# Optimization experiments

Measured on AMD Instinct MI355X. Metric: run time of the kernel, lower is better.

The kernel has to match this reference:

```python
import jax, jax.numpy as jnp
import numpy as np

EPS = 1e-5
NEG_SLOPE = 0.2

def _bn(x, gamma, beta):
    # BatchNorm1d in training mode: stats over (batch, length) per channel. x: [B,C,N]
    m = jnp.mean(x, axis=(0, 2), keepdims=True)
    v = jnp.mean((x - m) ** 2, axis=(0, 2), keepdims=True)  # biased variance
    return (x - m) * jax.lax.rsqrt(v + EPS) * gamma[None, :, None] + beta[None, :, None]

def setup_inputs() -> dict:
    key = jax.random.key(0)
    ks = jax.random.split(key, 7)
    B, C, N, H = 32, 64, 2048, 128
    s = 1.0 / np.sqrt(C)
    return {
        "x": jax.random.normal(ks[0], (B, C, N), dtype=jnp.float32),
        "wq": jax.random.normal(ks[1], (C, C), dtype=jnp.float32) * s,
        "wk": jax.random.normal(ks[2], (C, C), dtype=jnp.float32) * s,
        "wv": jax.random.normal(ks[3], (C, C), dtype=jnp.float32) * s,
        "w_ff1": jax.random.normal(ks[4], (H, C), dtype=jnp.float32) * s,
        "w_ff2": jax.random.normal(ks[5], (C, H), dtype=jnp.float32) * (1.0 / np.sqrt(H)),
        "bn1_gamma": jnp.ones((C,), dtype=jnp.float32),
        "bn1_beta": jnp.zeros((C,), dtype=jnp.float32),
        "bn2_gamma": jnp.ones((C,), dtype=jnp.float32),
        "bn2_beta": jnp.zeros((C,), dtype=jnp.float32),
    }

def reference(x, wq, wk, wv, w_ff1, w_ff2, bn1_gamma, bn1_beta, bn2_gamma, bn2_beta):
    # x: [B, C, N]; 1x1 convs are per-point channel matmuls
    C = x.shape[1]
    q = jnp.einsum('oc,bcn->bno', wq, x)          # [B,N,C]
    k = jnp.einsum('oc,bcn->bon', wk, x)          # [B,C,N]
    v = jnp.einsum('oc,bcn->bno', wv, x)          # [B,N,C] (v^T)
    energy = jnp.einsum('bnc,bcm->bnm', q, k)     # [B,N,N]
    attention = jax.nn.softmax(energy / jnp.sqrt(jnp.float32(C)), axis=-1)
    x_r = jnp.einsum('bnm,bmc->bcn', attention, v)  # [B,C,N]
    h = _bn(x + x_r, bn1_gamma, bn1_beta)
    ff = jnp.einsum('hc,bcn->bhn', w_ff1, h)      # [B,H,N]
    ff = jnp.where(ff >= 0, ff, NEG_SLOPE * ff)   # LeakyReLU(0.2)
    ff = jnp.einsum('ch,bhn->bcn', w_ff2, ff)     # [B,C,N]
    return _bn(h + ff, bn2_gamma, bn2_beta)
```

## Files before the change

### kernel.cpp

```cpp
#include <hip/hip_runtime.h>

#define B_ 32
#define C_ 64
#define N_ 2048
#define H_ 128

typedef unsigned short u16;
typedef unsigned int u32;
typedef float f32x4 __attribute__((ext_vector_type(4)));
typedef float f32x16 __attribute__((ext_vector_type(16)));
typedef __bf16 bf16x8 __attribute__((ext_vector_type(8)));
typedef __bf16 bf16x4 __attribute__((ext_vector_type(4)));
typedef unsigned short u16x4 __attribute__((ext_vector_type(4)));
typedef unsigned int u32x4v __attribute__((ext_vector_type(4)));

#define MFMA(a, b, c) __builtin_amdgcn_mfma_f32_16x16x32_bf16(a, b, c, 0, 0, 0)
#define MFMA32(a, b, c) __builtin_amdgcn_mfma_f32_32x32x16_bf16(a, b, c, 0, 0, 0)
#define EXP2(x) __builtin_amdgcn_exp2f(x)
#define LOG2E 1.44269504088896f

__device__ __forceinline__ int swz(int row, int cb) { return row * 128 + (cb ^ ((row & 7) << 4)); }
__device__ __forceinline__ int swz256(int row, int cb) { return row * 256 + (cb ^ ((row & 7) << 4)); }

__device__ __forceinline__ float b2f(u16 v) {
    union { u32 u; float f; } x; x.u = ((u32)v) << 16; return x.f;
}

__device__ __forceinline__ u32 cvtpk(float lo, float hi) {
    u32 r;
    asm("v_cvt_pk_bf16_f32 %0, %1, %2" : "=v"(r) : "v"(lo), "v"(hi));
    return r;
}

__device__ __forceinline__ bf16x8 pfrag(float p0, float p1, float p2, float p3,
                                        float p4, float p5, float p6, float p7) {
    u32 x1 = cvtpk(p0, p1), x2 = cvtpk(p2, p3);
    u32 y1 = cvtpk(p4, p5), y2 = cvtpk(p6, p7);
    asm volatile("v_permlane32_swap_b32 %0, %1" : "+v"(x1), "+v"(y1));
    asm volatile("v_permlane32_swap_b32 %0, %1" : "+v"(x2), "+v"(y2));
    u32x4v d; d[0] = x1; d[1] = x2; d[2] = y1; d[3] = y2;
    return __builtin_bit_cast(bf16x8, d);
}

__device__ __forceinline__ bf16x8 cvt8(const float* p, float s) {
    f32x4 a = *(const f32x4*)p, b = *(const f32x4*)(p + 4);
    bf16x8 o;
    o[0] = (__bf16)(a[0] * s); o[1] = (__bf16)(a[1] * s);
    o[2] = (__bf16)(a[2] * s); o[3] = (__bf16)(a[3] * s);
    o[4] = (__bf16)(b[0] * s); o[5] = (__bf16)(b[1] * s);
    o[6] = (__bf16)(b[2] * s); o[7] = (__bf16)(b[3] * s);
    return o;
}

__global__ __launch_bounds__(256) void qkv_k(
    const float* __restrict__ x,
    const float* __restrict__ wq, const float* __restrict__ wk, const float* __restrict__ wv,
    const float* __restrict__ w1, const float* __restrict__ w2,
    u16* __restrict__ Qg, u16* __restrict__ Kg, u16* __restrict__ Vg,
    u16* __restrict__ w1b, u16* __restrict__ w2b)
{
    const int b = blockIdx.y, nt = blockIdx.x, t = threadIdx.x;
    const int lane = t & 63, wave = t >> 6, g = lane >> 4, r16 = lane & 15;
    __shared__ __align__(16) u16 xT[128 * 64];
    const int n0 = nt * 128;

    bf16x8 wqf[4][2], wkf[4][2], wvf[4][2];
#pragma unroll
    for (int jt = 0; jt < 4; ++jt)
#pragma unroll
        for (int kc = 0; kc < 2; ++kc) {
            const int ro = (r16 + 16 * jt) * 64 + 8 * g + 32 * kc;
            wqf[jt][kc] = cvt8(wq + ro, 0.125f * LOG2E);
            wkf[jt][kc] = cvt8(wk + ro, 1.0f);
            wvf[jt][kc] = cvt8(wv + ro, 1.0f);
        }

    {
        int c = t >> 5;
        const int nn = (t & 31) * 4;
#pragma unroll
        for (int pass = 0; pass < 8; ++pass, c += 8) {
            f32x4 v = *(const f32x4*)&x[(size_t)(b * 64 + c) * 2048 + n0 + nn];
#pragma unroll
            for (int j = 0; j < 4; ++j)
                xT[swz(nn + j, 2 * c) >> 1] = __builtin_bit_cast(u16, (__bf16)v[j]);
        }
    }
    if (b == 0 && nt == 0) {
        for (int i = t; i < H_ * C_; i += 256) w1b[i] = __builtin_bit_cast(u16, (__bf16)w1[i]);
        for (int i = t; i < C_ * H_; i += 256) w2b[i] = __builtin_bit_cast(u16, (__bf16)w2[i]);
    }
    __syncthreads();

#pragma unroll
    for (int p = 0; p < 2; ++p) {
        const int nt16 = wave * 2 + p;
        bf16x8 xa[2];
#pragma unroll
        for (int kc = 0; kc < 2; ++kc)
            xa[kc] = *(const bf16x8*)&xT[swz(nt16 * 16 + r16, 16 * g + 64 * kc) >> 1];
#pragma unroll
        for (int jt = 0; jt < 4; ++jt) {
            f32x4 aq = {0.f, 0.f, 0.f, 0.f}, ak = {0.f, 0.f, 0.f, 0.f};
            aq = MFMA(wqf[jt][0], xa[0], aq); aq = MFMA(wqf[jt][1], xa[1], aq);
            ak = MFMA(wkf[jt][0], xa[0], ak); ak = MFMA(wkf[jt][1], xa[1], ak);
            bf16x4 qk, kk;
#pragma unroll
            for (int r = 0; r < 4; ++r) { qk[r] = (__bf16)aq[r]; kk[r] = (__bf16)ak[r]; }
            const size_t ro = (size_t)(b * 2048 + n0 + nt16 * 16 + r16) * 64 + 16 * jt + 4 * g;
            *(bf16x4*)&Qg[ro] = qk;
            *(bf16x4*)&Kg[ro] = kk;
        }
#pragma unroll
        for (int it = 0; it < 4; ++it) {
            f32x4 av = {0.f, 0.f, 0.f, 0.f};
            av = MFMA(xa[0], wvf[it][0], av);
            av = MFMA(xa[1], wvf[it][1], av);
            bf16x4 vk;
#pragma unroll
            for (int r = 0; r < 4; ++r) vk[r] = (__bf16)av[r];
            *(bf16x4*)&Vg[(size_t)(b * 64 + 16 * it + r16) * 2048 + n0 + nt16 * 16 + 4 * g] = vk;
        }
    }
}

__global__ __launch_bounds__(256) void attn_k(
    const u16* __restrict__ Qg, const u16* __restrict__ Kg, const u16* __restrict__ Vg,
    const float* __restrict__ x, u16* __restrict__ yb,
    float* __restrict__ ps, float* __restrict__ pq)
{
    const int t = threadIdx.x;
    const int lane = t & 63, wave = t >> 6, q = lane & 31, hi = lane >> 5;
    const int L = blockIdx.x;
    const int xcd = L & 7, slot = L >> 3;
    const int b = xcd * 4 + (slot >> 4);
    const int qt = slot & 15;

    __shared__ __align__(16) u16 Lds16[16384];
    char* lds = (char*)Lds16;

    const int n0 = qt * 128 + wave * 32;
    const int n = n0 + q;

    bf16x8 qf[4];
    {
        const u16* qrow = Qg + (size_t)(b * 2048 + n) * 64 + 8 * hi;
#pragma unroll
        for (int kc = 0; kc < 4; ++kc)
            qf[kc] = *(const bf16x8*)(qrow + 16 * kc);
    }

    f32x16 acc[2];
#pragma unroll
    for (int ct = 0; ct < 2; ++ct)
#pragma unroll
        for (int r = 0; r < 16; ++r) acc[ct][r] = 0.f;
    float m = -1e30f, lp = 0.f;

    const char* Kgb = (const char*)Kg + (size_t)b * 2048 * 128;
    const char* Vgb = (const char*)Vg + (size_t)b * 64 * 4096;
    const int srcxor = (((lane & 7) ^ (lane >> 3)) << 4);
    const int rowb = wave * 16 + (lane >> 3);

    auto stage = [&](int kvt, int buf) {
#pragma unroll
        for (int j = 0; j < 2; ++j) {
            const char* gk = Kgb + (size_t)(kvt * 64 + rowb + 8 * j) * 128 + srcxor;
            const char* gv = Vgb + (size_t)(rowb + 8 * j) * 4096 + kvt * 128 + srcxor;
            char* lk = lds + buf * 8192 + (wave * 2 + j) * 1024;
            __builtin_amdgcn_global_load_lds(
                (const __attribute__((address_space(1))) void*)gk,
                (__attribute__((address_space(3))) void*)lk, 16, 0, 0);
            __builtin_amdgcn_global_load_lds(
                (const __attribute__((address_space(1))) void*)gv,
                (__attribute__((address_space(3))) void*)(lk + 16384), 16, 0, 0);
        }
    };

    auto tile = [&](int kvt, int buf) {
        __syncthreads();
        if (kvt + 1 < 32) stage(kvt + 1, buf ^ 1);
        const char* Kc = lds + buf * 8192;
        const char* Vc = Kc + 16384;

        f32x16 st[2];
        __builtin_amdgcn_s_setprio(1);
#pragma unroll
        for (int it = 0; it < 2; ++it) {
            f32x16 a;
#pragma unroll
            for (int r = 0; r < 16; ++r) a[r] = 0.f;
#pragma unroll
            for (int kc = 0; kc < 4; ++kc) {
                bf16x8 kf = *(const bf16x8*)(Kc + swz(32 * it + q, 32 * kc + 16 * hi));
                a = MFMA32(kf, qf[kc], a);
            }
            st[it] = a;
        }
        __builtin_amdgcn_s_setprio(0);

        bf16x8 vf[2][4];
#pragma unroll
        for (int ct = 0; ct < 2; ++ct)
#pragma unroll
            for (int mc = 0; mc < 4; ++mc)
                vf[ct][mc] = *(const bf16x8*)(Vc + swz(32 * ct + q, 32 * mc + 16 * hi));

        float mx[2];
#pragma unroll
        for (int it = 0; it < 2; ++it) {
            float a0 = fmaxf(fmaxf(st[it][0], st[it][1]), fmaxf(st[it][2], st[it][3]));
            float a1 = fmaxf(fmaxf(st[it][4], st[it][5]), fmaxf(st[it][6], st[it][7]));
            float a2 = fmaxf(fmaxf(st[it][8], st[it][9]), fmaxf(st[it][10], st[it][11]));
            float a3 = fmaxf(fmaxf(st[it][12], st[it][13]), fmaxf(st[it][14], st[it][15]));
            mx[it] = fmaxf(fmaxf(a0, a1), fmaxf(a2, a3));
        }
        float pm = fmaxf(mx[0], mx[1]);
        pm = fmaxf(pm, __shfl_xor(pm, 32, 64));
        if (!__all(pm <= m + 8.f)) {
            const float mn = fmaxf(m, pm);
            const float al = EXP2(m - mn);
            m = mn; lp *= al;
#pragma unroll
            for (int ct = 0; ct < 2; ++ct)
#pragma unroll
                for (int r = 0; r < 16; ++r) acc[ct][r] *= al;
        }
        float ls = 0.f;
#pragma unroll
        for (int it = 0; it < 2; ++it) {
#pragma unroll
            for (int r = 0; r < 16; ++r) st[it][r] = EXP2(st[it][r] - m);
            float a0 = (st[it][0] + st[it][1]) + (st[it][2] + st[it][3]);
            float a1 = (st[it][4] + st[it][5]) + (st[it][6] + st[it][7]);
            float a2 = (st[it][8] + st[it][9]) + (st[it][10] + st[it][11]);
            float a3 = (st[it][12] + st[it][13]) + (st[it][14] + st[it][15]);
            ls += (a0 + a1) + (a2 + a3);
        }
        lp += ls;
        bf16x8 pf0 = pfrag(st[0][0], st[0][1], st[0][2], st[0][3],
                           st[0][4], st[0][5], st[0][6], st[0][7]);
        bf16x8 pf1 = pfrag(st[0][8], st[0][9], st[0][10], st[0][11],
                           st[0][12], st[0][13], st[0][14], st[0][15]);
        bf16x8 pf2 = pfrag(st[1][0], st[1][1], st[1][2], st[1][3],
                           st[1][4], st[1][5], st[1][6], st[1][7]);
        bf16x8 pf3 = pfrag(st[1][8], st[1][9], st[1][10], st[1][11],
                           st[1][12], st[1][13], st[1][14], st[1][15]);
        __builtin_amdgcn_s_setprio(1);
#pragma unroll
        for (int ct = 0; ct < 2; ++ct) {
            acc[ct] = MFMA32(vf[ct][0], pf0, acc[ct]);
            acc[ct] = MFMA32(vf[ct][1], pf1, acc[ct]);
            acc[ct] = MFMA32(vf[ct][2], pf2, acc[ct]);
            acc[ct] = MFMA32(vf[ct][3], pf3, acc[ct]);
        }
        __builtin_amdgcn_s_setprio(0);
    };

    stage(0, 0);
#pragma unroll 1
    for (int kvt = 0; kvt < 32; kvt += 2) {
        tile(kvt, 0);
        tile(kvt + 1, 1);
    }

    const float l = lp + __shfl_xor(lp, 32, 64);
    const float inv = 1.0f / l;
    float sv[2][16], qv[2][16];
#pragma unroll
    for (int ct = 0; ct < 2; ++ct)
#pragma unroll
        for (int r = 0; r < 16; ++r) {
            const int c = 32 * ct + (r & 3) + 8 * (r >> 2) + 4 * hi;
            const float o = acc[ct][r] * inv + x[(size_t)(b * 64 + c) * 2048 + n];
            sv[ct][r] = o;
            qv[ct][r] = o * o;
        }
#pragma unroll
    for (int ct = 0; ct < 2; ++ct)
#pragma unroll
        for (int grp = 0; grp < 4; ++grp) {
            bf16x4 ov;
#pragma unroll
            for (int r = 0; r < 4; ++r) ov[r] = (__bf16)sv[ct][4 * grp + r];
            *(bf16x4*)&yb[(size_t)(b * 2048 + n) * 64 + 32 * ct + 8 * grp + 4 * hi] = ov;
        }
#pragma unroll
    for (int d = 1; d <= 16; d <<= 1)
#pragma unroll
        for (int ct = 0; ct < 2; ++ct)
#pragma unroll
            for (int r = 0; r < 16; ++r) {
                sv[ct][r] += __shfl_xor(sv[ct][r], d, 64);
                qv[ct][r] += __shfl_xor(qv[ct][r], d, 64);
            }
    __syncthreads();
    float* sb = (float*)lds;
    if (q == 0) {
#pragma unroll
        for (int ct = 0; ct < 2; ++ct)
#pragma unroll
            for (int r = 0; r < 16; ++r) {
                const int c = 32 * ct + (r & 3) + 8 * (r >> 2) + 4 * hi;
                sb[wave * 64 + c] = sv[ct][r];
                sb[256 + wave * 64 + c] = qv[ct][r];
            }
    }
    __syncthreads();
    if (t < 64) {
        ps[L * 64 + t] = sb[t] + sb[64 + t] + sb[128 + t] + sb[192 + t];
        pq[L * 64 + t] = sb[256 + t] + sb[320 + t] + sb[384 + t] + sb[448 + t];
    }
}

__global__ __launch_bounds__(256) void finalize_k(
    const float* __restrict__ psum, const float* __restrict__ psq,
    const float* __restrict__ gamma, const float* __restrict__ beta,
    float* __restrict__ ss, int nblk)
{
    const int c = blockIdx.x, t = threadIdx.x;
    const int lane = t & 63, wave = t >> 6;
    float s = 0.f, q = 0.f;
    for (int bl = t; bl < nblk; bl += 256) {
        s += psum[bl * 64 + c];
        q += psq[bl * 64 + c];
    }
#pragma unroll
    for (int d = 1; d <= 32; d <<= 1) {
        s += __shfl_xor(s, d, 64);
        q += __shfl_xor(q, d, 64);
    }
    __shared__ float ls[4], lq[4];
    if (lane == 0) { ls[wave] = s; lq[wave] = q; }
    __syncthreads();
    if (t == 0) {
        s = ls[0] + ls[1] + ls[2] + ls[3];
        q = lq[0] + lq[1] + lq[2] + lq[3];
        const float mean = s * (1.0f / 65536.0f);
        const float var  = q * (1.0f / 65536.0f) - mean * mean;
        const float sc   = rsqrtf(var + 1e-5f) * gamma[c];
        ss[c] = sc;
        ss[64 + c] = beta[c] - mean * sc;
    }
}

__global__ __launch_bounds__(256) void ff_k(
    const u16* __restrict__ y, const float* __restrict__ ss1,
    const u16* __restrict__ w1b, const u16* __restrict__ w2b,
    u16* __restrict__ zb, float* __restrict__ ps, float* __restrict__ pq)
{
    const int b = blockIdx.y, nt = blockIdx.x, t = threadIdx.x;
    const int lane = t & 63, wave = t >> 6, g = lane >> 4, r16 = lane & 15;
    const int L = blockIdx.y * gridDim.x + blockIdx.x;
    __shared__ __align__(16) u16 hT[64 * 64];
    __shared__ __align__(16) float hf[64 * 68];
    __shared__ __align__(16) u16 pb[4][16 * 128];
    __shared__ float sc1[64], sh1[64];
    if (t < 64) { sc1[t] = ss1[t]; sh1[t] = ss1[64 + t]; }
    __syncthreads();
    const int n0 = nt * 64;
    {
        const int i = t >> 2, c0 = (t & 3) * 16;
        u16 yb16[16] __attribute__((aligned(16)));
        *(uint4*)&yb16[0] = *(const uint4*)&y[(size_t)(b * 2048 + n0 + i) * 64 + c0];
        *(uint4*)&yb16[8] = *(const uint4*)&y[(size_t)(b * 2048 + n0 + i) * 64 + c0 + 8];
        u16 hb[16] __attribute__((aligned(16)));
#pragma unroll
        for (int j = 0; j < 16; ++j) {
            const int c = c0 + j;
            const float hv = b2f(yb16[j]) * sc1[c] + sh1[c];
            hf[i * 68 + c] = hv;
            hb[j] = __builtin_bit_cast(u16, (__bf16)hv);
        }
        *(uint4*)&hT[swz(i, 2 * c0) >> 1]      = *(const uint4*)&hb[0];
        *(uint4*)&hT[swz(i, 2 * c0 + 16) >> 1] = *(const uint4*)&hb[8];
    }
    __syncthreads();

    bf16x8 ha[2];
#pragma unroll
    for (int kc = 0; kc < 2; ++kc)
        ha[kc] = *(const bf16x8*)&hT[swz(wave * 16 + r16, 16 * g + 64 * kc) >> 1];
#pragma unroll
    for (int it = 0; it < 8; ++it) {
        f32x4 a = {0.f, 0.f, 0.f, 0.f};
#pragma unroll
        for (int kc = 0; kc < 2; ++kc) {
            bf16x8 w1f = *(const bf16x8*)&w1b[(r16 + 16 * it) * 64 + 8 * g + 32 * kc];
            a = MFMA(w1f, ha[kc], a);
        }
        u16x4 pk;
#pragma unroll
        for (int r = 0; r < 4; ++r) {
            const float rv = a[r] >= 0.f ? a[r] : 0.2f * a[r];
            pk[r] = __builtin_bit_cast(u16, (__bf16)rv);
        }
        *(u16x4*)&pb[wave][swz256(r16, 2 * (16 * it + 4 * g)) >> 1] = pk;
    }
    bf16x8 pa[4];
#pragma unroll
    for (int kc = 0; kc < 4; ++kc)
        pa[kc] = *(const bf16x8*)&pb[wave][swz256(r16, 16 * g + 64 * kc) >> 1];
    const int nl = wave * 16 + r16;
    float sv[4][4], qv[4][4];
#pragma unroll
    for (int jt = 0; jt < 4; ++jt) {
        f32x4 a = {0.f, 0.f, 0.f, 0.f};
#pragma unroll
        for (int kc = 0; kc < 4; ++kc) {
            bf16x8 w2f = *(const bf16x8*)&w2b[(r16 + 16 * jt) * 128 + 8 * g + 32 * kc];
            a = MFMA(w2f, pa[kc], a);
        }
        f32x4 h4 = *(const f32x4*)&hf[nl * 68 + 16 * jt + 4 * g];
        bf16x4 zk;
#pragma unroll
        for (int r = 0; r < 4; ++r) {
            a[r] += h4[r];
            sv[jt][r] = a[r];
            qv[jt][r] = a[r] * a[r];
            zk[r] = (__bf16)a[r];
        }
        *(bf16x4*)&zb[(size_t)(b * 2048 + n0 + nl) * 64 + 16 * jt + 4 * g] = zk;
    }
#pragma unroll
    for (int d = 1; d <= 8; d <<= 1)
#pragma unroll
        for (int jt = 0; jt < 4; ++jt)
#pragma unroll
            for (int r = 0; r < 4; ++r) {
                sv[jt][r] += __shfl_xor(sv[jt][r], d, 64);
                qv[jt][r] += __shfl_xor(qv[jt][r], d, 64);
            }
    __syncthreads();
    float* sb = (float*)&pb[0][0];
    if (r16 == 0) {
#pragma unroll
        for (int jt = 0; jt < 4; ++jt)
#pragma unroll
            for (int r = 0; r < 4; ++r) {
                const int c = 16 * jt + 4 * g + r;
                sb[wave * 64 + c] = sv[jt][r];
                sb[256 + wave * 64 + c] = qv[jt][r];
            }
    }
    __syncthreads();
    if (t < 64) {
        ps[L * 64 + t] = sb[t] + sb[64 + t] + sb[128 + t] + sb[192 + t];
        pq[L * 64 + t] = sb[256 + t] + sb[320 + t] + sb[384 + t] + sb[448 + t];
    }
}

__global__ __launch_bounds__(256) void bnout_k(
    const u16* __restrict__ zb, const float* __restrict__ ss2, float* __restrict__ out)
{
    const int b = blockIdx.y, nt = blockIdx.x, t = threadIdx.x;
    __shared__ float tile[64 * 65];
    __shared__ float sc2[64], sh2[64];
    if (t < 64) { sc2[t] = ss2[t]; sh2[t] = ss2[64 + t]; }
    __syncthreads();
    const int n0 = nt * 64;
    {
        const int i = t >> 2, c0 = (t & 3) * 16;
        u16 zb16[16] __attribute__((aligned(16)));
        *(uint4*)&zb16[0] = *(const uint4*)&zb[(size_t)(b * 2048 + n0 + i) * 64 + c0];
        *(uint4*)&zb16[8] = *(const uint4*)&zb[(size_t)(b * 2048 + n0 + i) * 64 + c0 + 8];
#pragma unroll
        for (int j = 0; j < 16; ++j) {
            const int c = c0 + j;
            tile[i * 65 + c] = b2f(zb16[j]) * sc2[c] + sh2[c];
        }
    }
    __syncthreads();
    {
        const int c = t >> 2, j0 = (t & 3) * 16;
#pragma unroll
        for (int q4 = 0; q4 < 4; ++q4) {
            f32x4 ov;
#pragma unroll
            for (int j = 0; j < 4; ++j)
                ov[j] = tile[(j0 + 4 * q4 + j) * 65 + c];
            *(f32x4*)&out[(size_t)(b * 64 + c) * 2048 + n0 + j0 + 4 * q4] = ov;
        }
    }
}

extern "C" void kernel_launch(void* const* d_in, const int* in_sizes, int n_in,
                              void* d_out, int out_size, void* d_ws, size_t ws_size,
                              hipStream_t stream)
{
    const float* x   = (const float*)d_in[0];
    const float* wq  = (const float*)d_in[1];
    const float* wk  = (const float*)d_in[2];
    const float* wv  = (const float*)d_in[3];
    const float* w1  = (const float*)d_in[4];
    const float* w2  = (const float*)d_in[5];
    const float* g1  = (const float*)d_in[6];
    const float* be1 = (const float*)d_in[7];
    const float* g2  = (const float*)d_in[8];
    const float* be2 = (const float*)d_in[9];
    float* out = (float*)d_out;

    char* w = (char*)d_ws;
    u16* Qg = (u16*)w;   w += (size_t)B_ * N_ * C_ * 2;
    u16* Kg = (u16*)w;   w += (size_t)B_ * N_ * C_ * 2;
    u16* Vg = (u16*)w;   w += (size_t)B_ * N_ * C_ * 2;
    u16* yb = (u16*)w;   w += (size_t)B_ * N_ * C_ * 2;
    u16* zb = (u16*)w;   w += (size_t)B_ * N_ * C_ * 2;
    u16* w1b = (u16*)w;  w += (size_t)H_ * C_ * 2;
    u16* w2b = (u16*)w;  w += (size_t)C_ * H_ * 2;
    float* ps1 = (float*)w; w += 1024 * 64 * 4;
    float* pq1 = (float*)w; w += 1024 * 64 * 4;
    float* ps2 = (float*)w; w += 1024 * 64 * 4;
    float* pq2 = (float*)w; w += 1024 * 64 * 4;
    float* ss1 = (float*)w; w += 128 * 4;
    float* ss2 = (float*)w; w += 128 * 4;

    const dim3 blk(256);
    hipLaunchKernelGGL(qkv_k,   dim3(16, 32), blk, 0, stream, x, wq, wk, wv, w1, w2, Qg, Kg, Vg, w1b, w2b);
    hipLaunchKernelGGL(attn_k,  dim3(512),    blk, 0, stream, Qg, Kg, Vg, x, yb, ps1, pq1);
    hipLaunchKernelGGL(finalize_k, dim3(64),  blk, 0, stream, ps1, pq1, g1, be1, ss1, 512);
    hipLaunchKernelGGL(ff_k,    dim3(32, 32), blk, 0, stream, yb, ss1, w1b, w2b, zb, ps2, pq2);
    hipLaunchKernelGGL(finalize_k, dim3(64),  blk, 0, stream, ps2, pq2, g2, be2, ss2, 1024);
    hipLaunchKernelGGL(bnout_k, dim3(32, 32), blk, 0, stream, zb, ss2, out);
}
```

Before: 127.5 us.

## Load V fragments directly from global memory and vectorize LDS stores in BN kernels

The attention kernel no longer stages V tiles through LDS with async global-to-LDS loads. Each lane now reads its V fragments straight from global memory at the top of each tile, which halves LDS use and may raise occupancy. In exchange the V reads no longer go through the double-buffered prefetch, so global latency lands inside the loop and the per-lane reads are strided rather than coalesced. Separately, the FFN and bnout kernels store their normalized values to LDS as 128-bit vectors, and the bnout tile stride goes from 65 to 68.

Result: slower. 144.7 us (+13.5%).

```diff
diff --git a/kernel.cpp b/kernel.cpp
--- a/kernel.cpp
+++ b/kernel.cpp
@@ -136,7 +136,7 @@
     const int b = xcd * 4 + (slot >> 4);
     const int qt = slot & 15;
 
-    __shared__ __align__(16) u16 Lds16[16384];
+    __shared__ __align__(16) u16 Lds16[8192];
     char* lds = (char*)Lds16;
 
     const int n0 = qt * 128 + wave * 32;
@@ -158,7 +158,7 @@
     float m = -1e30f, lp = 0.f;
 
     const char* Kgb = (const char*)Kg + (size_t)b * 2048 * 128;
-    const char* Vgb = (const char*)Vg + (size_t)b * 64 * 4096;
+    const char* Vl = (const char*)Vg + ((size_t)(b * 64 + q)) * 4096 + 16 * hi;
     const int srcxor = (((lane & 7) ^ (lane >> 3)) << 4);
     const int rowb = wave * 16 + (lane >> 3);
 
@@ -166,14 +166,10 @@
 #pragma unroll
         for (int j = 0; j < 2; ++j) {
             const char* gk = Kgb + (size_t)(kvt * 64 + rowb + 8 * j) * 128 + srcxor;
-            const char* gv = Vgb + (size_t)(rowb + 8 * j) * 4096 + kvt * 128 + srcxor;
             char* lk = lds + buf * 8192 + (wave * 2 + j) * 1024;
             __builtin_amdgcn_global_load_lds(
                 (const __attribute__((address_space(1))) void*)gk,
                 (__attribute__((address_space(3))) void*)lk, 16, 0, 0);
-            __builtin_amdgcn_global_load_lds(
-                (const __attribute__((address_space(1))) void*)gv,
-                (__attribute__((address_space(3))) void*)(lk + 16384), 16, 0, 0);
         }
     };
 
@@ -181,7 +177,14 @@
         __syncthreads();
         if (kvt + 1 < 32) stage(kvt + 1, buf ^ 1);
         const char* Kc = lds + buf * 8192;
-        const char* Vc = Kc + 16384;
+
+        bf16x8 vf[2][4];
+        const char* Vt = Vl + kvt * 128;
+#pragma unroll
+        for (int ct = 0; ct < 2; ++ct)
+#pragma unroll
+            for (int mc = 0; mc < 4; ++mc)
+                vf[ct][mc] = *(const bf16x8*)(Vt + ct * 131072 + mc * 32);
 
         f32x16 st[2];
         __builtin_amdgcn_s_setprio(1);
@@ -198,13 +201,6 @@
             st[it] = a;
         }
         __builtin_amdgcn_s_setprio(0);
-
-        bf16x8 vf[2][4];
-#pragma unroll
-        for (int ct = 0; ct < 2; ++ct)
-#pragma unroll
-            for (int mc = 0; mc < 4; ++mc)
-                vf[ct][mc] = *(const bf16x8*)(Vc + swz(32 * ct + q, 32 * mc + 16 * hi));
 
         float mx[2];
 #pragma unroll
@@ -366,11 +362,15 @@
         *(uint4*)&yb16[8] = *(const uint4*)&y[(size_t)(b * 2048 + n0 + i) * 64 + c0 + 8];
         u16 hb[16] __attribute__((aligned(16)));
 #pragma unroll
-        for (int j = 0; j < 16; ++j) {
-            const int c = c0 + j;
-            const float hv = b2f(yb16[j]) * sc1[c] + sh1[c];
-            hf[i * 68 + c] = hv;
-            hb[j] = __builtin_bit_cast(u16, (__bf16)hv);
+        for (int q4 = 0; q4 < 4; ++q4) {
+            f32x4 hv;
+#pragma unroll
+            for (int j = 0; j < 4; ++j) {
+                const int c = c0 + 4 * q4 + j;
+                hv[j] = b2f(yb16[4 * q4 + j]) * sc1[c] + sh1[c];
+                hb[4 * q4 + j] = __builtin_bit_cast(u16, (__bf16)hv[j]);
+            }
+            *(f32x4*)&hf[i * 68 + c0 + 4 * q4] = hv;
         }
         *(uint4*)&hT[swz(i, 2 * c0) >> 1]      = *(const uint4*)&hb[0];
         *(uint4*)&hT[swz(i, 2 * c0 + 16) >> 1] = *(const uint4*)&hb[8];
@@ -454,7 +454,7 @@
     const u16* __restrict__ zb, const float* __restrict__ ss2, float* __restrict__ out)
 {
     const int b = blockIdx.y, nt = blockIdx.x, t = threadIdx.x;
-    __shared__ float tile[64 * 65];
+    __shared__ float tile[64 * 68];
     __shared__ float sc2[64], sh2[64];
     if (t < 64) { sc2[t] = ss2[t]; sh2[t] = ss2[64 + t]; }
     __syncthreads();
@@ -465,9 +465,14 @@
         *(uint4*)&zb16[0] = *(const uint4*)&zb[(size_t)(b * 2048 + n0 + i) * 64 + c0];
         *(uint4*)&zb16[8] = *(const uint4*)&zb[(size_t)(b * 2048 + n0 + i) * 64 + c0 + 8];
 #pragma unroll
-        for (int j = 0; j < 16; ++j) {
-            const int c = c0 + j;
-            tile[i * 65 + c] = b2f(zb16[j]) * sc2[c] + sh2[c];
+        for (int q4 = 0; q4 < 4; ++q4) {
+            f32x4 tv;
+#pragma unroll
+            for (int j = 0; j < 4; ++j) {
+                const int c = c0 + 4 * q4 + j;
+                tv[j] = b2f(zb16[4 * q4 + j]) * sc2[c] + sh2[c];
+            }
+            *(f32x4*)&tile[i * 68 + c0 + 4 * q4] = tv;
         }
     }
     __syncthreads();
@@ -478,7 +483,7 @@
             f32x4 ov;
 #pragma unroll
             for (int j = 0; j < 4; ++j)
-                ov[j] = tile[(j0 + 4 * q4 + j) * 65 + c];
+                ov[j] = tile[(j0 + 4 * q4 + j) * 68 + c];
             *(f32x4*)&out[(size_t)(b * 64 + c) * 2048 + n0 + j0 + 4 * q4] = ov;
         }
     }
```
